# Optimization experiments

Measured on AMD Instinct MI355X. Metric: run time of the kernel, lower is better.

The kernel has to match this reference:

```python
import jax, jax.numpy as jnp
import numpy as np

N = 50000       # nodes
E = 800000      # edges (before self-loops)
G = 512         # graphs in batch
IN_DIM = 128
OUT_DIM = 8
DIMS = [(IN_DIM, 32), (32, 64), (64, 128), (128, 64)]
EPS = 1e-5


def setup_inputs() -> dict:
    key = jax.random.key(0)
    ks = jax.random.split(key, 40)
    def nrm(k, shape, s=0.05):
        return jax.random.normal(k, shape, jnp.float32) * s
    inp = {}
    inp["x"] = jax.random.normal(ks[0], (N, IN_DIM), jnp.float32)
    inp["edge_index"] = jax.random.randint(ks[1], (2, E), 0, N, dtype=jnp.int32)
    inp["batch"] = jnp.sort(jax.random.randint(ks[2], (N,), 0, G, dtype=jnp.int32))
    for i, (din, dout) in enumerate(DIMS, 1):
        inp[f"W{i}"]  = nrm(ks[3 * i + 0], (din, dout))
        inp[f"as{i}"] = nrm(ks[3 * i + 1], (dout,))
        inp[f"ad{i}"] = nrm(ks[3 * i + 2], (dout,))
        inp[f"b{i}"]  = jnp.zeros((dout,), jnp.float32)
        inp[f"g{i}"]  = jnp.ones((dout,), jnp.float32)   # BN gamma
        inp[f"be{i}"] = jnp.zeros((dout,), jnp.float32)  # BN beta
    inp["Wf"] = nrm(ks[20], (64, 32)); inp["bf"] = jnp.zeros((32,), jnp.float32)
    inp["Wc"] = nrm(ks[21], (32, OUT_DIM)); inp["bc"] = jnp.zeros((OUT_DIM,), jnp.float32)
    return inp


def gat_conv(x, src, dst, W, a_s, a_d, b):
    """PyG GATConv, heads=1: linear (no bias) -> per-edge attention with
    leaky_relu(0.2) -> segment softmax over incoming edges -> scatter-add -> bias."""
    h = x @ W                                   # [N, F]
    a_src = h @ a_s                             # [N]
    a_dst = h @ a_d                             # [N]
    e = jax.nn.leaky_relu(a_src[src] + a_dst[dst], 0.2)   # [E+N]
    m = jax.ops.segment_max(e, dst, num_segments=N)
    w = jnp.exp(e - m[dst])
    denom = jax.ops.segment_sum(w, dst, num_segments=N)
    alpha = w / denom[dst]                      # self-loops guarantee denom > 0
    out = jax.ops.segment_sum(alpha[:, None] * h[src], dst, num_segments=N)
    return out + b


def batch_norm(x, g, be):
    mu = x.mean(axis=0)
    var = x.var(axis=0)                         # biased, as torch training BN
    return (x - mu) * jax.lax.rsqrt(var + EPS) * g + be


def reference(x, edge_index, batch,
              W1, as1, ad1, b1, g1, be1,
              W2, as2, ad2, b2, g2, be2,
              W3, as3, ad3, b3, g3, be3,
              W4, as4, ad4, b4, g4, be4,
              Wf, bf, Wc, bc):
    loops = jnp.arange(N, dtype=edge_index.dtype)
    src = jnp.concatenate([edge_index[0], loops])   # GATConv adds self-loops
    dst = jnp.concatenate([edge_index[1], loops])
    params = [(W1, as1, ad1, b1, g1, be1), (W2, as2, ad2, b2, g2, be2),
              (W3, as3, ad3, b3, g3, be3), (W4, as4, ad4, b4, g4, be4)]
    h = x
    for (W, a_s, a_d, b, g, be) in params:
        h = jax.nn.leaky_relu(gat_conv(h, src, dst, W, a_s, a_d, b), 0.01)
        h = batch_norm(h, g, be)
    pooled = jax.ops.segment_sum(h, batch, num_segments=G)   # global_add_pool
    z = jax.nn.leaky_relu(pooled @ Wf + bf, 0.01)
    return jax.nn.sigmoid(z @ Wc + bc)
```

## Files before the change

### kernel.cpp

```cpp
#include <hip/hip_runtime.h>
#include <math.h>

constexpr int BLK = 256;
constexpr int NBLKA = 256;
constexpr int NSH = 16;

static inline int cdiv(long a, long b) { return (int)((a + b - 1) / b); }

typedef __attribute__((ext_vector_type(8))) short short8;
typedef __attribute__((ext_vector_type(4))) float floatx4;

__device__ __forceinline__ unsigned short f2bf(float f) {
    unsigned u = __float_as_uint(f);
    unsigned r = u + 0x7fffu + ((u >> 16) & 1u);
    return (unsigned short)(r >> 16);
}
__device__ __forceinline__ float bf2f(unsigned short s) {
    return __uint_as_float(((unsigned)s) << 16);
}


__global__ void histA_k(const int* __restrict__ dst, int* __restrict__ histg,
                        int E, int nbkt, int chunk) {
    __shared__ int h[256];
    int tid = threadIdx.x, z = blockIdx.x;
    h[tid] = 0;
    __syncthreads();
    int e0 = z * chunk, e1 = min(E, e0 + chunk);
    for (int e = e0 + tid; e < e1; e += BLK) atomicAdd(&h[dst[e] >> 8], 1);
    __syncthreads();
    if (tid < nbkt) histg[z * nbkt + tid] = h[tid];
}

__global__ void blk_scan2_k(int* __restrict__ histg, int* __restrict__ bsum, int nbkt) {
    __shared__ int s[BLK];
    int t = threadIdx.x, b = blockIdx.x;
    int v = histg[t * nbkt + b];
    s[t] = v;
    __syncthreads();
    for (int o = 1; o < BLK; o <<= 1) {
        int tv = (t >= o) ? s[t - o] : 0;
        __syncthreads();
        s[t] += tv;
        __syncthreads();
    }
    histg[t * nbkt + b] = s[t] - v;
    if (t == BLK - 1) bsum[b] = s[t];
}

__global__ void scan_base_k(const int* __restrict__ bsum, int* __restrict__ bucket_base,
                            int nbkt, int E, int* __restrict__ gs, int* __restrict__ ge,
                            int G, float* __restrict__ bnstats) {
    __shared__ int s[BLK];
    int t = threadIdx.x;
    int v = (t < nbkt) ? bsum[t] : 0;
    s[t] = v;
    __syncthreads();
    for (int o = 1; o < BLK; o <<= 1) {
        int tv = (t >= o) ? s[t - o] : 0;
        __syncthreads();
        s[t] += tv;
        __syncthreads();
    }
    if (t < nbkt) bucket_base[t] = s[t] - v;
    if (t == 0) bucket_base[nbkt] = E;
    for (int i = t; i < G; i += BLK) { gs[i] = 0x7fffffff; ge[i] = -1; }
    for (int i = t; i < 4 * NSH * 256; i += BLK) bnstats[i] = 0.f;
}

__global__ void csrB_k(const unsigned* __restrict__ ebkt, const int* __restrict__ bucket_base,
                       int* __restrict__ off, unsigned short* __restrict__ csr,
                       const int* __restrict__ batch, int* __restrict__ gs,
                       int* __restrict__ ge, int N, int E, int nbkt) {
    __shared__ int dg[256];
    __shared__ int sc[256];
    int t = threadIdx.x, b = blockIdx.x;
    int n0 = b << 8;
    int cnt = min(256, N - n0);
    dg[t] = (t < cnt) ? 1 : 0;
    __syncthreads();
    int e0 = bucket_base[b], e1 = bucket_base[b + 1];
    for (int e = e0 + t; e < e1; e += BLK) atomicAdd(&dg[ebkt[e] >> 16], 1);
    __syncthreads();
    int d = dg[t];
    sc[t] = d;
    __syncthreads();
    for (int o = 1; o < BLK; o <<= 1) {
        int tv = (t >= o) ? sc[t - o] : 0;
        __syncthreads();
        sc[t] += tv;
        __syncthreads();
    }
    int loff = sc[t] - d;
    int csrbase = e0 + n0;
    if (t < cnt) {
        off[n0 + t] = csrbase + loff;
        csr[csrbase + loff] = (unsigned short)(n0 + t);
        dg[t] = loff + 1;
    }
    if (b == nbkt - 1 && t == 0) off[N] = E + N;
    int n = n0 + t;
    if (n < N) {
        int bb = batch[n];
        if (n == 0) gs[bb] = 0;
        else {
            int pb = batch[n - 1];
            if (pb != bb) { gs[bb] = n; ge[pb] = n - 1; }
        }
        if (n == N - 1) ge[bb] = N - 1;
    }
    __syncthreads();
    for (int e = e0 + t; e < e1; e += BLK) {
        unsigned w = ebkt[e];
        int pos = atomicAdd(&dg[w >> 16], 1);
        csr[csrbase + pos] = (unsigned short)(w & 0xffff);
    }
}

template <int K, int NOUT, bool AFP32, bool HASBN>
__device__ __forceinline__ void gemm_body(int bx, const void* __restrict__ av,
                           const float* __restrict__ W,
                           const float* __restrict__ a_s, const float* __restrict__ a_d,
                           const float* __restrict__ bnst, const float* __restrict__ g_prev,
                           const float* __restrict__ be_prev, float invN,
                           unsigned short* __restrict__ hb,
                           float* __restrict__ asrc, float* __restrict__ adst, int N) {
    constexpr int KF = K / 32;
    constexpr int NY = NOUT / 16;
    __shared__ float s_sca[K], s_scc[K], s_rs[K], s_rd[K], s_bd[2];
    int tid = threadIdx.x;
    if (tid < K) {
        float a = 1.f, c = 0.f;
        if (HASBN) {
            float su = 0.f, sq = 0.f;
#pragma unroll
            for (int s = 0; s < NSH; ++s) {
                su += bnst[s * 256 + tid];
                sq += bnst[s * 256 + 128 + tid];
            }
            float mu = su * invN;
            float var = sq * invN - mu * mu;
            a = g_prev[tid] * rsqrtf(var + 1e-5f);
            c = be_prev[tid] - mu * a;
        }
        s_sca[tid] = a; s_scc[tid] = c;
    }
    __syncthreads();
    {
        if (tid < K) {
            const float* wr = W + (long)tid * NOUT;
            float rs = 0.f, rd = 0.f;
            for (int f = 0; f < NOUT; ++f) {
                float w = wr[f];
                rs += w * a_s[f];
                rd += w * a_d[f];
            }
            s_rs[tid] = rs; s_rd[tid] = rd;
        }
        __syncthreads();
        if (tid < 2) {
            const float* r = tid ? s_rd : s_rs;
            float b = 0.f;
            for (int k = 0; k < K; ++k) b += s_scc[k] * r[k];
            s_bd[tid] = b;
        }
        __syncthreads();
    }

    int wave = tid >> 6;
    int lane = tid & 63;
    int quad = lane >> 4;
    int r16 = lane & 15;
    int blockbase = bx * 128;

    short8 afr[2][KF];
    bool valid[2];
#pragma unroll
    for (int rt = 0; rt < 2; ++rt) {
        int tilebase = blockbase + wave * 32 + rt * 16;
        valid[rt] = tilebase < N;
        if (!valid[rt]) continue;
        int arow = min(tilebase + r16, N - 1);
        if (AFP32) {
            const float* xr = (const float*)av + (long)arow * K;
#pragma unroll
            for (int kk = 0; kk < KF; ++kk) {
                float4 x0 = *(const float4*)(xr + kk * 32 + quad * 8);
                float4 x1 = *(const float4*)(xr + kk * 32 + quad * 8 + 4);
                short8 a;
                a[0] = (short)f2bf(x0.x); a[1] = (short)f2bf(x0.y);
                a[2] = (short)f2bf(x0.z); a[3] = (short)f2bf(x0.w);
                a[4] = (short)f2bf(x1.x); a[5] = (short)f2bf(x1.y);
                a[6] = (short)f2bf(x1.z); a[7] = (short)f2bf(x1.w);
                afr[rt][kk] = a;
            }
        } else {
            const unsigned short* hr = (const unsigned short*)av + (long)arow * K;
#pragma unroll
            for (int kk = 0; kk < KF; ++kk)
                afr[rt][kk] = *(const short8*)(hr + kk * 32 + quad * 8);
        }
        float ds = 0.f, dd = 0.f;
#pragma unroll
        for (int kk = 0; kk < KF; ++kk) {
            int kb = kk * 32 + quad * 8;
#pragma unroll
            for (int j = 0; j < 8; ++j) {
                int k = kb + j;
                float a = bf2f((unsigned short)afr[rt][kk][j]) * s_sca[k];
                ds += a * s_rs[k];
                dd += a * s_rd[k];
            }
        }
        ds += __shfl_xor(ds, 16, 64); ds += __shfl_xor(ds, 32, 64);
        dd += __shfl_xor(dd, 16, 64); dd += __shfl_xor(dd, 32, 64);
        int drow = tilebase + r16;
        if (quad == 0 && drow < N) {
            asrc[drow] = ds + s_bd[0];
            adst[drow] = dd + s_bd[1];
        }
    }

#pragma unroll
    for (int y = 0; y < NY; ++y) {
        int col = y * 16 + r16;
        short8 bfr[KF];
        float biasp = 0.f;
#pragma unroll
        for (int kk = 0; kk < KF; ++kk) {
            short8 b;
#pragma unroll
            for (int j = 0; j < 8; ++j) {
                int k = kk * 32 + quad * 8 + j;
                float w = W[(long)k * NOUT + col];
                b[j] = (short)f2bf(s_sca[k] * w);
                biasp += s_scc[k] * w;
            }
            bfr[kk] = b;
        }
        biasp += __shfl_xor(biasp, 16, 64);
        biasp += __shfl_xor(biasp, 32, 64);

#pragma unroll
        for (int rt = 0; rt < 2; ++rt) {
            if (!valid[rt]) continue;
            int tilebase = blockbase + wave * 32 + rt * 16;
            floatx4 acc = {0.f, 0.f, 0.f, 0.f};
#pragma unroll
            for (int kk = 0; kk < KF; ++kk)
                acc = __builtin_amdgcn_mfma_f32_16x16x32_bf16(afr[rt][kk], bfr[kk], acc, 0, 0, 0);
#pragma unroll
            for (int rr = 0; rr < 4; ++rr) {
                int srow = tilebase + quad * 4 + rr;
                if (srow < N) hb[(long)srow * NOUT + col] = f2bf(acc[rr] + biasp);
            }
        }
    }
}

template <int K, int NOUT, bool AFP32, bool HASBN>
__launch_bounds__(256)
__global__ void gemm_fused(const void* __restrict__ av, const float* __restrict__ W,
                           const float* __restrict__ a_s, const float* __restrict__ a_d,
                           const float* __restrict__ bnst, const float* __restrict__ g_prev,
                           const float* __restrict__ be_prev, float invN,
                           unsigned short* __restrict__ hb,
                           float* __restrict__ asrc, float* __restrict__ adst, int N) {
    gemm_body<K, NOUT, AFP32, HASBN>(blockIdx.x, av, W, a_s, a_d, bnst, g_prev, be_prev,
                                     invN, hb, asrc, adst, N);
}

__launch_bounds__(256)
__global__ void scatter_gemm0_k(const int* __restrict__ src, const int* __restrict__ dst,
                                const int* __restrict__ histg, const int* __restrict__ bucket_base,
                                unsigned* __restrict__ ebkt, int E, int nbkt, int chunk,
                                const float* __restrict__ x, const float* __restrict__ W0,
                                const float* __restrict__ as0, const float* __restrict__ ad0,
                                unsigned short* __restrict__ hb,
                                float* __restrict__ asrc, float* __restrict__ adst, int N) {
    if (blockIdx.x < NBLKA) {
        __shared__ int cur[256];
        int tid = threadIdx.x, z = blockIdx.x;
        if (tid < nbkt) cur[tid] = histg[z * nbkt + tid] + bucket_base[tid];
        __syncthreads();
        int e0 = z * chunk, e1 = min(E, e0 + chunk);
        for (int e = e0 + tid; e < e1; e += BLK) {
            int d = dst[e];
            int b = d >> 8;
            int pos = atomicAdd(&cur[b], 1);
            ebkt[pos] = ((unsigned)(d & 255) << 16) | (unsigned)src[e];
        }
    } else {
        gemm_body<128, 32, true, false>(blockIdx.x - NBLKA, x, W0, as0, ad0,
                                        nullptr, nullptr, nullptr, 0.f, hb, asrc, adst, N);
    }
}

template <int DOUT, int FPL>
__global__ void gather_fused(const int* __restrict__ off,
                             const unsigned short* __restrict__ csr,
                             const float* __restrict__ asrc, const float* __restrict__ adst,
                             const unsigned short* __restrict__ hb,
                             const float* __restrict__ b,
                             unsigned short* __restrict__ out,
                             float* __restrict__ bn, int N) {
    constexpr int TPN = DOUT / FPL;
    constexpr int NV = FPL / 8;
    __shared__ float sst[2 * DOUT];
    int tid = threadIdx.x;
    if (tid < 2 * DOUT) sst[tid] = 0.f;
    __syncthreads();

    int t = blockIdx.x * blockDim.x + tid;
    int d = t / TPN;
    int l = t % TPN;
    bool active = d < N;
    int lane = tid & 63;

    int p0 = 0, p1 = 0;
    float ad = 0.f;
    if (active) { p0 = off[d]; p1 = off[d + 1]; ad = adst[d]; }
    const int f0 = l * FPL;

    float acc[FPL];
#pragma unroll
    for (int i = 0; i < FPL; ++i) acc[i] = 0.f;
    float sum = 0.f;

#pragma unroll 4
    for (int p = p0; p < p1; ++p) {
        int s = csr[p];
        float e = asrc[s] + ad;
        e = e > 0.f ? e : 0.2f * e;
        float w = __expf(e);
        sum += w;
        const unsigned short* hr = hb + (long)s * DOUT + f0;
#pragma unroll
        for (int v = 0; v < NV; ++v) {
            const uint4 hv = *(const uint4*)(hr + v * 8);
            acc[v * 8 + 0] += w * bf2f((unsigned short)(hv.x & 0xffff));
            acc[v * 8 + 1] += w * bf2f((unsigned short)(hv.x >> 16));
            acc[v * 8 + 2] += w * bf2f((unsigned short)(hv.y & 0xffff));
            acc[v * 8 + 3] += w * bf2f((unsigned short)(hv.y >> 16));
            acc[v * 8 + 4] += w * bf2f((unsigned short)(hv.z & 0xffff));
            acc[v * 8 + 5] += w * bf2f((unsigned short)(hv.z >> 16));
            acc[v * 8 + 6] += w * bf2f((unsigned short)(hv.w & 0xffff));
            acc[v * 8 + 7] += w * bf2f((unsigned short)(hv.w >> 16));
        }
    }
    float inv = active ? (1.f / sum) : 0.f;

#pragma unroll
    for (int v = 0; v < NV; ++v) {
        float4 b0 = *(const float4*)(b + f0 + v * 8);
        float4 b1 = *(const float4*)(b + f0 + v * 8 + 4);
        float bbv[8] = {b0.x, b0.y, b0.z, b0.w, b1.x, b1.y, b1.z, b1.w};
        unsigned pk[4];
#pragma unroll
        for (int i = 0; i < 4; ++i) {
            float v0 = acc[v * 8 + 2 * i] * inv + bbv[2 * i];
            float v1 = acc[v * 8 + 2 * i + 1] * inv + bbv[2 * i + 1];
            v0 = v0 > 0.f ? v0 : 0.01f * v0;
            v1 = v1 > 0.f ? v1 : 0.01f * v1;
            if (!active) { v0 = 0.f; v1 = 0.f; }
            acc[v * 8 + 2 * i] = v0;
            acc[v * 8 + 2 * i + 1] = v1;
            pk[i] = (unsigned)f2bf(v0) | ((unsigned)f2bf(v1) << 16);
        }
        if (active)
            *(uint4*)(out + (long)d * DOUT + f0 + v * 8) = uint4{pk[0], pk[1], pk[2], pk[3]};
    }

#pragma unroll
    for (int i = 0; i < FPL; ++i) {
        float s = acc[i];
        float q = s * s;
#pragma unroll
        for (int o = TPN; o < 64; o <<= 1) {
            s += __shfl_xor(s, o, 64);
            q += __shfl_xor(q, o, 64);
        }
        if (lane < TPN) {
            atomicAdd(&sst[f0 + i], s);
            atomicAdd(&sst[DOUT + f0 + i], q);
        }
    }
    __syncthreads();
    if (tid < 2 * DOUT) {
        float* base = bn + (blockIdx.x & (NSH - 1)) * 256;
        int idx = (tid < DOUT) ? tid : (128 + tid - DOUT);
        atomicAdd(&base[idx], sst[tid]);
    }
}

__global__ void pool_head_k(const unsigned short* __restrict__ h, const int* __restrict__ gs,
                            const int* __restrict__ ge, const float* __restrict__ bnst,
                            const float* __restrict__ g4, const float* __restrict__ be4,
                            float invN, const float* __restrict__ Wf,
                            const float* __restrict__ bf, const float* __restrict__ Wc,
                            const float* __restrict__ bc, float* __restrict__ out) {
    int g = blockIdx.x;
    int t = threadIdx.x;
    int f = t & 63, sub = t >> 6;
    __shared__ float pp[4][64];
    __shared__ float p[64];
    __shared__ float z[32];
    int s0 = gs[g], s1 = ge[g];
    float acc = 0.f;
    if (s0 <= s1)
        for (int n = s0 + sub; n <= s1; n += 4) acc += bf2f(h[(long)n * 64 + f]);
    pp[sub][f] = acc;
    __syncthreads();
    if (t < 64) {
        float su = 0.f, sq = 0.f;
#pragma unroll
        for (int s = 0; s < NSH; ++s) {
            su += bnst[s * 256 + t];
            sq += bnst[s * 256 + 128 + t];
        }
        float mu = su * invN;
        float var = sq * invN - mu * mu;
        float a = g4[t] * rsqrtf(var + 1e-5f);
        float c = be4[t] - mu * a;
        float cnt = (s0 <= s1) ? (float)(s1 - s0 + 1) : 0.f;
        p[t] = a * (pp[0][t] + pp[1][t] + pp[2][t] + pp[3][t]) + cnt * c;
    }
    __syncthreads();
    if (t < 32) {
        float zacc = bf[t];
#pragma unroll
        for (int ff = 0; ff < 64; ++ff) zacc += p[ff] * Wf[ff * 32 + t];
        z[t] = zacc > 0.f ? zacc : 0.01f * zacc;
    }
    __syncthreads();
    if (t < 8) {
        float oacc = bc[t];
#pragma unroll
        for (int o = 0; o < 32; ++o) oacc += z[o] * Wc[o * 8 + t];
        out[(long)g * 8 + t] = 1.f / (1.f + __expf(-oacc));
    }
}

extern "C" void kernel_launch(void* const* d_in, const int* in_sizes, int n_in,
                              void* d_out, int out_size, void* d_ws, size_t ws_size,
                              hipStream_t stream) {
    const float* x   = (const float*)d_in[0];
    const int* ei    = (const int*)d_in[1];
    const int* batch = (const int*)d_in[2];
    const int N  = in_sizes[2];
    const int E  = in_sizes[1] / 2;
    const int ET = E + N;
    const int G  = out_size / 8;
    const int* src = ei;
    const int* dst = ei + E;

    const float *W[4], *as_[4], *ad_[4], *bb[4], *gg[4], *be_[4];
    for (int i = 0; i < 4; ++i) {
        W[i]   = (const float*)d_in[3 + 6 * i];
        as_[i] = (const float*)d_in[4 + 6 * i];
        ad_[i] = (const float*)d_in[5 + 6 * i];
        bb[i]  = (const float*)d_in[6 + 6 * i];
        gg[i]  = (const float*)d_in[7 + 6 * i];
        be_[i] = (const float*)d_in[8 + 6 * i];
    }
    const float* Wf = (const float*)d_in[27];
    const float* bfp = (const float*)d_in[28];
    const float* Wc = (const float*)d_in[29];
    const float* bc = (const float*)d_in[30];

    float* ws = (float*)d_ws;
    long off_ = 0;
    auto alloc = [&](long nelem) { float* p = ws + off_; off_ += (nelem + 3) & ~3L; return p; };
    unsigned short* h2a = (unsigned short*)alloc((long)N * 64);
    unsigned short* h2b = (unsigned short*)alloc((long)N * 64);
    unsigned short* hb  = (unsigned short*)alloc((long)N * 64);
    float* asrc     = alloc(N);
    float* adst     = alloc(N);
    float* bnstats  = alloc((long)4 * NSH * 256);
    unsigned* ebkt  = (unsigned*)alloc(E);
    int* histg      = (int*)alloc((long)NBLKA * 256);
    int* bucket_base = (int*)alloc(260);
    int* bsum       = (int*)alloc(256);
    int* off        = (int*)alloc(N + 1);
    unsigned short* csr = (unsigned short*)alloc(ET / 2 + 2);
    int* gs         = (int*)alloc(G);
    int* ge         = (int*)alloc(G);
    (void)ws_size; (void)n_in;

    const int nbkt = cdiv(N, 256);
    const int chunk = cdiv(E, NBLKA);
    const float invN = 1.f / (float)N;

    histA_k<<<NBLKA, BLK, 0, stream>>>(dst, histg, E, nbkt, chunk);
    blk_scan2_k<<<nbkt, BLK, 0, stream>>>(histg, bsum, nbkt);
    scan_base_k<<<1, BLK, 0, stream>>>(bsum, bucket_base, nbkt, E, gs, ge, G, bnstats);
    scatter_gemm0_k<<<NBLKA + cdiv(N, 128), BLK, 0, stream>>>(
        src, dst, histg, bucket_base, ebkt, E, nbkt, chunk,
        x, W[0], as_[0], ad_[0], hb, asrc, adst, N);
    csrB_k<<<nbkt, BLK, 0, stream>>>(ebkt, bucket_base, off, csr, batch, gs, ge, N, E, nbkt);

    gather_fused<32, 8><<<cdiv((long)N * 4, BLK), BLK, 0, stream>>>(
        off, csr, asrc, adst, hb, bb[0], h2b, bnstats + 0L * NSH * 256, N);

#define LAYER(i, DIN, DOUT, FPL, INP, OUTP, BNPREV, GPREV, BEPREV)                        \
    do {                                                                                  \
        gemm_fused<DIN, DOUT, false, true>                                                \
            <<<cdiv(N, 128), 256, 0, stream>>>(                                           \
                INP, W[i], as_[i], ad_[i], BNPREV, GPREV, BEPREV, invN,                   \
                hb, asrc, adst, N);                                                       \
        gather_fused<DOUT, FPL><<<cdiv((long)N * (DOUT / FPL), BLK), BLK, 0, stream>>>(   \
            off, csr, asrc, adst, hb, bb[i], OUTP, bnstats + (long)i * NSH * 256, N);     \
    } while (0)

    LAYER(1, 32,  64, 16, h2b, h2a, bnstats + 0L * NSH * 256, gg[0], be_[0]);
    LAYER(2, 64, 128, 16, h2a, h2b, bnstats + 1L * NSH * 256, gg[1], be_[1]);
    LAYER(3, 128, 64, 16, h2b, h2a, bnstats + 2L * NSH * 256, gg[2], be_[2]);
#undef LAYER

    pool_head_k<<<G, 256, 0, stream>>>(h2a, gs, ge, bnstats + 3L * NSH * 256, gg[3], be_[3],
                                       invN, Wf, bfp, Wc, bc, (float*)d_out);
}
```

Before: 346.6 us.

## Aggregate before transform for expanding GAT layers, fuse BN stats into GEMM

For layers 1 and 2, where output width exceeds input width, the raw normalized-free input features are gathered and aggregated over incoming edges first, and the linear transform (with folded BN scale/shift, bias, leaky ReLU and BN statistics) is applied afterwards. This relies on the attention weights summing to one so that the BN shift passes through the aggregation. A separate dots kernel computes the attention logits directly from the input features, and the gather gains a non-finalizing variant. The gather now moves 32- or 64-wide rows instead of 64- or 128-wide ones, at the cost of extra kernel launches and the BN reduction moving into the GEMM. The gather loop unroll also drops from 4 to 2.

```diff
diff --git a/kernel.cpp b/kernel.cpp
--- a/kernel.cpp
+++ b/kernel.cpp
@@ -117,18 +117,23 @@
     }
 }
 
-template <int K, int NOUT, bool AFP32, bool HASBN>
+template <int K, int NOUT, bool AFP32, bool HASBN, bool DOTS, bool FIN>
 __device__ __forceinline__ void gemm_body(int bx, const void* __restrict__ av,
                            const float* __restrict__ W,
                            const float* __restrict__ a_s, const float* __restrict__ a_d,
                            const float* __restrict__ bnst, const float* __restrict__ g_prev,
                            const float* __restrict__ be_prev, float invN,
+                           const float* __restrict__ bias_l,
                            unsigned short* __restrict__ hb,
-                           float* __restrict__ asrc, float* __restrict__ adst, int N) {
+                           float* __restrict__ asrc, float* __restrict__ adst,
+                           float* __restrict__ bn_out, int N) {
     constexpr int KF = K / 32;
     constexpr int NY = NOUT / 16;
-    __shared__ float s_sca[K], s_scc[K], s_rs[K], s_rd[K], s_bd[2];
+    __shared__ float s_sca[K], s_scc[K];
+    __shared__ float s_rs[DOTS ? K : 1], s_rd[DOTS ? K : 1], s_bd[2];
+    __shared__ float sst[FIN ? 2 * NOUT : 1];
     int tid = threadIdx.x;
+    if (FIN && tid < 2 * NOUT) sst[tid] = 0.f;
     if (tid < K) {
         float a = 1.f, c = 0.f;
         if (HASBN) {
@@ -144,10 +149,7 @@
             c = be_prev[tid] - mu * a;
         }
         s_sca[tid] = a; s_scc[tid] = c;
-    }
-    __syncthreads();
-    {
-        if (tid < K) {
+        if (DOTS) {
             const float* wr = W + (long)tid * NOUT;
             float rs = 0.f, rd = 0.f;
             for (int f = 0; f < NOUT; ++f) {
@@ -157,7 +159,9 @@
             }
             s_rs[tid] = rs; s_rd[tid] = rd;
         }
-        __syncthreads();
+    }
+    __syncthreads();
+    if constexpr (DOTS) {
         if (tid < 2) {
             const float* r = tid ? s_rd : s_rs;
             float b = 0.f;
@@ -200,24 +204,26 @@
             for (int kk = 0; kk < KF; ++kk)
                 afr[rt][kk] = *(const short8*)(hr + kk * 32 + quad * 8);
         }
-        float ds = 0.f, dd = 0.f;
-#pragma unroll
-        for (int kk = 0; kk < KF; ++kk) {
-            int kb = kk * 32 + quad * 8;
-#pragma unroll
-            for (int j = 0; j < 8; ++j) {
-                int k = kb + j;
-                float a = bf2f((unsigned short)afr[rt][kk][j]) * s_sca[k];
-                ds += a * s_rs[k];
-                dd += a * s_rd[k];
-            }
-        }
-        ds += __shfl_xor(ds, 16, 64); ds += __shfl_xor(ds, 32, 64);
-        dd += __shfl_xor(dd, 16, 64); dd += __shfl_xor(dd, 32, 64);
-        int drow = tilebase + r16;
-        if (quad == 0 && drow < N) {
-            asrc[drow] = ds + s_bd[0];
-            adst[drow] = dd + s_bd[1];
+        if constexpr (DOTS) {
+            float ds = 0.f, dd = 0.f;
+#pragma unroll
+            for (int kk = 0; kk < KF; ++kk) {
+                int kb = kk * 32 + quad * 8;
+#pragma unroll
+                for (int j = 0; j < 8; ++j) {
+                    int k = kb + j;
+                    float a = bf2f((unsigned short)afr[rt][kk][j]) * s_sca[k];
+                    ds += a * s_rs[k];
+                    dd += a * s_rd[k];
+                }
+            }
+            ds += __shfl_xor(ds, 16, 64); ds += __shfl_xor(ds, 32, 64);
+            dd += __shfl_xor(dd, 16, 64); dd += __shfl_xor(dd, 32, 64);
+            int drow = tilebase + r16;
+            if (quad == 0 && drow < N) {
+                asrc[drow] = ds + s_bd[0];
+                adst[drow] = dd + s_bd[1];
+            }
         }
     }
 
@@ -240,7 +246,9 @@
         }
         biasp += __shfl_xor(biasp, 16, 64);
         biasp += __shfl_xor(biasp, 32, 64);
-
+        if (FIN) biasp += bias_l[col];
+
+        float sS = 0.f, sQ = 0.f;
 #pragma unroll
         for (int rt = 0; rt < 2; ++rt) {
             if (!valid[rt]) continue;
@@ -252,22 +260,48 @@
 #pragma unroll
             for (int rr = 0; rr < 4; ++rr) {
                 int srow = tilebase + quad * 4 + rr;
-                if (srow < N) hb[(long)srow * NOUT + col] = f2bf(acc[rr] + biasp);
-            }
-        }
-    }
-}
-
-template <int K, int NOUT, bool AFP32, bool HASBN>
+                if (srow < N) {
+                    float v = acc[rr] + biasp;
+                    if (FIN) {
+                        v = v > 0.f ? v : 0.01f * v;
+                        sS += v; sQ += v * v;
+                    }
+                    hb[(long)srow * NOUT + col] = f2bf(v);
+                }
+            }
+        }
+        if constexpr (FIN) {
+            sS += __shfl_xor(sS, 16, 64); sS += __shfl_xor(sS, 32, 64);
+            sQ += __shfl_xor(sQ, 16, 64); sQ += __shfl_xor(sQ, 32, 64);
+            if (quad == 0) {
+                atomicAdd(&sst[col], sS);
+                atomicAdd(&sst[NOUT + col], sQ);
+            }
+        }
+    }
+    if constexpr (FIN) {
+        __syncthreads();
+        if (tid < 2 * NOUT) {
+            float* base = bn_out + (bx & (NSH - 1)) * 256;
+            int idx = (tid < NOUT) ? tid : (128 + tid - NOUT);
+            atomicAdd(&base[idx], sst[tid]);
+        }
+    }
+}
+
+template <int K, int NOUT, bool AFP32, bool HASBN, bool DOTS, bool FIN>
 __launch_bounds__(256)
 __global__ void gemm_fused(const void* __restrict__ av, const float* __restrict__ W,
                            const float* __restrict__ a_s, const float* __restrict__ a_d,
                            const float* __restrict__ bnst, const float* __restrict__ g_prev,
                            const float* __restrict__ be_prev, float invN,
+                           const float* __restrict__ bias_l,
                            unsigned short* __restrict__ hb,
-                           float* __restrict__ asrc, float* __restrict__ adst, int N) {
-    gemm_body<K, NOUT, AFP32, HASBN>(blockIdx.x, av, W, a_s, a_d, bnst, g_prev, be_prev,
-                                     invN, hb, asrc, adst, N);
+                           float* __restrict__ asrc, float* __restrict__ adst,
+                           float* __restrict__ bn_out, int N) {
+    gemm_body<K, NOUT, AFP32, HASBN, DOTS, FIN>(blockIdx.x, av, W, a_s, a_d, bnst, g_prev,
+                                                be_prev, invN, bias_l, hb, asrc, adst,
+                                                bn_out, N);
 }
 
 __launch_bounds__(256)
@@ -291,12 +325,68 @@
             ebkt[pos] = ((unsigned)(d & 255) << 16) | (unsigned)src[e];
         }
     } else {
-        gemm_body<128, 32, true, false>(blockIdx.x - NBLKA, x, W0, as0, ad0,
-                                        nullptr, nullptr, nullptr, 0.f, hb, asrc, adst, N);
-    }
-}
-
-template <int DOUT, int FPL>
+        gemm_body<128, 32, true, false, true, false>(blockIdx.x - NBLKA, x, W0, as0, ad0,
+                                                     nullptr, nullptr, nullptr, 0.f, nullptr,
+                                                     hb, asrc, adst, nullptr, N);
+    }
+}
+
+template <int K, int NOUT>
+__global__ void dots_k(const unsigned short* __restrict__ y, const float* __restrict__ W,
+                       const float* __restrict__ a_s, const float* __restrict__ a_d,
+                       const float* __restrict__ bnst, const float* __restrict__ g_prev,
+                       const float* __restrict__ be_prev, float invN,
+                       float* __restrict__ asrc, float* __restrict__ adst, int N) {
+    __shared__ float crs[K], crd[K], s_scc[K], s_rs[K], s_rd[K], bd[2];
+    int tid = threadIdx.x;
+    if (tid < K) {
+        float su = 0.f, sq = 0.f;
+#pragma unroll
+        for (int s = 0; s < NSH; ++s) {
+            su += bnst[s * 256 + tid];
+            sq += bnst[s * 256 + 128 + tid];
+        }
+        float mu = su * invN;
+        float var = sq * invN - mu * mu;
+        float a = g_prev[tid] * rsqrtf(var + 1e-5f);
+        float c = be_prev[tid] - mu * a;
+        const float* wr = W + (long)tid * NOUT;
+        float rs = 0.f, rd = 0.f;
+        for (int f = 0; f < NOUT; ++f) {
+            float w = wr[f];
+            rs += w * a_s[f];
+            rd += w * a_d[f];
+        }
+        crs[tid] = a * rs; crd[tid] = a * rd;
+        s_scc[tid] = c; s_rs[tid] = rs; s_rd[tid] = rd;
+    }
+    __syncthreads();
+    if (tid < 2) {
+        const float* r = tid ? s_rd : s_rs;
+        float b = 0.f;
+        for (int k = 0; k < K; ++k) b += s_scc[k] * r[k];
+        bd[tid] = b;
+    }
+    __syncthreads();
+    int n = blockIdx.x * blockDim.x + tid;
+    if (n >= N) return;
+    const unsigned short* yr = y + (long)n * K;
+    float ds = bd[0], dd = bd[1];
+#pragma unroll
+    for (int kk = 0; kk < K / 8; ++kk) {
+        short8 v8 = *(const short8*)(yr + kk * 8);
+#pragma unroll
+        for (int j = 0; j < 8; ++j) {
+            float yv = bf2f((unsigned short)v8[j]);
+            ds += yv * crs[kk * 8 + j];
+            dd += yv * crd[kk * 8 + j];
+        }
+    }
+    asrc[n] = ds;
+    adst[n] = dd;
+}
+
+template <int DOUT, int FPL, bool FIN>
 __global__ void gather_fused(const int* __restrict__ off,
                              const unsigned short* __restrict__ csr,
                              const float* __restrict__ asrc, const float* __restrict__ adst,
@@ -306,10 +396,12 @@
                              float* __restrict__ bn, int N) {
     constexpr int TPN = DOUT / FPL;
     constexpr int NV = FPL / 8;
-    __shared__ float sst[2 * DOUT];
+    __shared__ float sst[FIN ? 2 * DOUT : 1];
     int tid = threadIdx.x;
-    if (tid < 2 * DOUT) sst[tid] = 0.f;
-    __syncthreads();
+    if constexpr (FIN) {
+        if (tid < 2 * DOUT) sst[tid] = 0.f;
+        __syncthreads();
+    }
 
     int t = blockIdx.x * blockDim.x + tid;
     int d = t / TPN;
@@ -327,7 +419,7 @@
     for (int i = 0; i < FPL; ++i) acc[i] = 0.f;
     float sum = 0.f;
 
-#pragma unroll 4
+#pragma unroll 2
     for (int p = p0; p < p1; ++p) {
         int s = csr[p];
         float e = asrc[s] + ad;
@@ -350,46 +442,63 @@
     }
     float inv = active ? (1.f / sum) : 0.f;
 
-#pragma unroll
-    for (int v = 0; v < NV; ++v) {
-        float4 b0 = *(const float4*)(b + f0 + v * 8);
-        float4 b1 = *(const float4*)(b + f0 + v * 8 + 4);
-        float bbv[8] = {b0.x, b0.y, b0.z, b0.w, b1.x, b1.y, b1.z, b1.w};
-        unsigned pk[4];
-#pragma unroll
-        for (int i = 0; i < 4; ++i) {
-            float v0 = acc[v * 8 + 2 * i] * inv + bbv[2 * i];
-            float v1 = acc[v * 8 + 2 * i + 1] * inv + bbv[2 * i + 1];
-            v0 = v0 > 0.f ? v0 : 0.01f * v0;
-            v1 = v1 > 0.f ? v1 : 0.01f * v1;
-            if (!active) { v0 = 0.f; v1 = 0.f; }
-            acc[v * 8 + 2 * i] = v0;
-            acc[v * 8 + 2 * i + 1] = v1;
-            pk[i] = (unsigned)f2bf(v0) | ((unsigned)f2bf(v1) << 16);
-        }
-        if (active)
-            *(uint4*)(out + (long)d * DOUT + f0 + v * 8) = uint4{pk[0], pk[1], pk[2], pk[3]};
-    }
-
-#pragma unroll
-    for (int i = 0; i < FPL; ++i) {
-        float s = acc[i];
-        float q = s * s;
-#pragma unroll
-        for (int o = TPN; o < 64; o <<= 1) {
-            s += __shfl_xor(s, o, 64);
-            q += __shfl_xor(q, o, 64);
-        }
-        if (lane < TPN) {
-            atomicAdd(&sst[f0 + i], s);
-            atomicAdd(&sst[DOUT + f0 + i], q);
-        }
-    }
-    __syncthreads();
-    if (tid < 2 * DOUT) {
-        float* base = bn + (blockIdx.x & (NSH - 1)) * 256;
-        int idx = (tid < DOUT) ? tid : (128 + tid - DOUT);
-        atomicAdd(&base[idx], sst[tid]);
+    if constexpr (!FIN) {
+        if (active) {
+#pragma unroll
+            for (int v = 0; v < NV; ++v) {
+                unsigned pk[4];
+#pragma unroll
+                for (int i = 0; i < 4; ++i) {
+                    float v0 = acc[v * 8 + 2 * i] * inv;
+                    float v1 = acc[v * 8 + 2 * i + 1] * inv;
+                    pk[i] = (unsigned)f2bf(v0) | ((unsigned)f2bf(v1) << 16);
+                }
+                *(uint4*)(out + (long)d * DOUT + f0 + v * 8) = uint4{pk[0], pk[1], pk[2], pk[3]};
+            }
+        }
+        return;
+    } else {
+#pragma unroll
+        for (int v = 0; v < NV; ++v) {
+            float4 b0 = *(const float4*)(b + f0 + v * 8);
+            float4 b1 = *(const float4*)(b + f0 + v * 8 + 4);
+            float bbv[8] = {b0.x, b0.y, b0.z, b0.w, b1.x, b1.y, b1.z, b1.w};
+            unsigned pk[4];
+#pragma unroll
+            for (int i = 0; i < 4; ++i) {
+                float v0 = acc[v * 8 + 2 * i] * inv + bbv[2 * i];
+                float v1 = acc[v * 8 + 2 * i + 1] * inv + bbv[2 * i + 1];
+                v0 = v0 > 0.f ? v0 : 0.01f * v0;
+                v1 = v1 > 0.f ? v1 : 0.01f * v1;
+                if (!active) { v0 = 0.f; v1 = 0.f; }
+                acc[v * 8 + 2 * i] = v0;
+                acc[v * 8 + 2 * i + 1] = v1;
+                pk[i] = (unsigned)f2bf(v0) | ((unsigned)f2bf(v1) << 16);
+            }
+            if (active)
+                *(uint4*)(out + (long)d * DOUT + f0 + v * 8) = uint4{pk[0], pk[1], pk[2], pk[3]};
+        }
+
+#pragma unroll
+        for (int i = 0; i < FPL; ++i) {
+            float s = acc[i];
+            float q = s * s;
+#pragma unroll
+            for (int o = TPN; o < 64; o <<= 1) {
+                s += __shfl_xor(s, o, 64);
+                q += __shfl_xor(q, o, 64);
+            }
+            if (lane < TPN) {
+                atomicAdd(&sst[f0 + i], s);
+                atomicAdd(&sst[DOUT + f0 + i], q);
+            }
+        }
+        __syncthreads();
+        if (tid < 2 * DOUT) {
+            float* base = bn + (blockIdx.x & (NSH - 1)) * 256;
+            int idx = (tid < DOUT) ? tid : (128 + tid - DOUT);
+            atomicAdd(&base[idx], sst[tid]);
+        }
     }
 }
 
@@ -490,6 +599,10 @@
     const int nbkt = cdiv(N, 256);
     const int chunk = cdiv(E, NBLKA);
     const float invN = 1.f / (float)N;
+    float* bn0 = bnstats + 0L * NSH * 256;
+    float* bn1 = bnstats + 1L * NSH * 256;
+    float* bn2 = bnstats + 2L * NSH * 256;
+    float* bn3 = bnstats + 3L * NSH * 256;
 
     histA_k<<<NBLKA, BLK, 0, stream>>>(dst, histg, E, nbkt, chunk);
     blk_scan2_k<<<nbkt, BLK, 0, stream>>>(histg, bsum, nbkt);
@@ -499,24 +612,31 @@
         x, W[0], as_[0], ad_[0], hb, asrc, adst, N);
     csrB_k<<<nbkt, BLK, 0, stream>>>(ebkt, bucket_base, off, csr, batch, gs, ge, N, E, nbkt);
 
-    gather_fused<32, 8><<<cdiv((long)N * 4, BLK), BLK, 0, stream>>>(
-        off, csr, asrc, adst, hb, bb[0], h2b, bnstats + 0L * NSH * 256, N);
-
-#define LAYER(i, DIN, DOUT, FPL, INP, OUTP, BNPREV, GPREV, BEPREV)                        \
-    do {                                                                                  \
-        gemm_fused<DIN, DOUT, false, true>                                                \
-            <<<cdiv(N, 128), 256, 0, stream>>>(                                           \
-                INP, W[i], as_[i], ad_[i], BNPREV, GPREV, BEPREV, invN,                   \
-                hb, asrc, adst, N);                                                       \
-        gather_fused<DOUT, FPL><<<cdiv((long)N * (DOUT / FPL), BLK), BLK, 0, stream>>>(   \
-            off, csr, asrc, adst, hb, bb[i], OUTP, bnstats + (long)i * NSH * 256, N);     \
-    } while (0)
-
-    LAYER(1, 32,  64, 16, h2b, h2a, bnstats + 0L * NSH * 256, gg[0], be_[0]);
-    LAYER(2, 64, 128, 16, h2a, h2b, bnstats + 1L * NSH * 256, gg[1], be_[1]);
-    LAYER(3, 128, 64, 16, h2b, h2a, bnstats + 2L * NSH * 256, gg[2], be_[2]);
-#undef LAYER
-
-    pool_head_k<<<G, 256, 0, stream>>>(h2a, gs, ge, bnstats + 3L * NSH * 256, gg[3], be_[3],
+    gather_fused<32, 8, true><<<cdiv((long)N * 4, BLK), BLK, 0, stream>>>(
+        off, csr, asrc, adst, hb, bb[0], h2b, bn0, N);
+
+    dots_k<32, 64><<<cdiv(N, BLK), BLK, 0, stream>>>(
+        h2b, W[1], as_[1], ad_[1], bn0, gg[0], be_[0], invN, asrc, adst, N);
+    gather_fused<32, 8, false><<<cdiv((long)N * 4, BLK), BLK, 0, stream>>>(
+        off, csr, asrc, adst, h2b, nullptr, hb, nullptr, N);
+    gemm_fused<32, 64, false, true, false, true><<<cdiv(N, 128), 256, 0, stream>>>(
+        hb, W[1], nullptr, nullptr, bn0, gg[0], be_[0], invN, bb[1], h2a,
+        nullptr, nullptr, bn1, N);
+
+    dots_k<64, 128><<<cdiv(N, BLK), BLK, 0, stream>>>(
+        h2a, W[2], as_[2], ad_[2], bn1, gg[1], be_[1], invN, asrc, adst, N);
+    gather_fused<64, 16, false><<<cdiv((long)N * 4, BLK), BLK, 0, stream>>>(
+        off, csr, asrc, adst, h2a, nullptr, hb, nullptr, N);
+    gemm_fused<64, 128, false, true, false, true><<<cdiv(N, 128), 256, 0, stream>>>(
+        hb, W[2], nullptr, nullptr, bn1, gg[1], be_[1], invN, bb[2], h2b,
+        nullptr, nullptr, bn2, N);
+
+    gemm_fused<128, 64, false, true, true, false><<<cdiv(N, 128), 256, 0, stream>>>(
+        h2b, W[3], as_[3], ad_[3], bn2, gg[2], be_[2], invN, nullptr, hb,
+        asrc, adst, nullptr, N);
+    gather_fused<64, 16, true><<<cdiv((long)N * 4, BLK), BLK, 0, stream>>>(
+        off, csr, asrc, adst, hb, bb[3], h2a, bn3, N);
+
+    pool_head_k<<<G, 256, 0, stream>>>(h2a, gs, ge, bn3, gg[3], be_[3],
                                        invN, Wf, bfp, Wc, bc, (float*)d_out);
 }
```

Result: faster. 315.4 us (-9.0%).
